# Kernel optimization log

Hardware: AMD Instinct MI355X
Metric: run time of the kernel (lower is better)

## Reference

```python
import jax, jax.numpy as jnp
import numpy as np

NUM_CLASSES = 345
EPS = 1e-12  # torch F.normalize eps


def setup_inputs() -> dict:
    key = jax.random.key(0)
    k1, k2, k3, k4 = jax.random.split(key, 4)
    B, D, N, C = 65536, 512, 34500, NUM_CLASSES
    z = jax.random.normal(k1, (B, D), dtype=jnp.float32)
    supports = jax.random.normal(k2, (N, D), dtype=jnp.float32)
    ent = jax.random.uniform(k3, (N,), dtype=jnp.float32)
    y_hat = jax.random.randint(k4, (N,), 0, C, dtype=jnp.int32)
    return {"z": z, "supports": supports, "ent": ent, "y_hat": y_hat, "filter_K": 100}


def reference(z, supports, ent, y_hat, filter_K):
    # Per-class top-filter_K selection by lowest entropy, expressed as a mask:
    # globally stable-sort by entropy, then per-class running count via one-hot cumsum.
    C = NUM_CLASSES
    order = jnp.argsort(ent)                      # stable sort -> matches per-class torch.sort tie-break
    y_sorted = y_hat[order]                       # [N]
    onehot = jax.nn.one_hot(y_sorted, C, dtype=z.dtype)  # [N, C]
    # rank (1-based, within own class) of each sorted support
    rank = jnp.sum(jnp.cumsum(onehot, axis=0) * onehot, axis=1)  # [N]
    sel = (rank <= filter_K).astype(z.dtype)      # [N] selection mask

    sup = supports[order]                         # [N, D]
    sup = sup / jnp.maximum(jnp.linalg.norm(sup, axis=1, keepdims=True), EPS)  # row-normalize
    # weights = selected_supports^T @ selected_labels (selection folded into mask)
    weights = jnp.einsum('nd,nc->dc', sup, onehot * sel[:, None])  # [D, C]
    weights = weights / jnp.maximum(jnp.linalg.norm(weights, axis=0, keepdims=True), EPS)
    return z @ weights                            # [B, C]
```

## Files before the change

### kernel.cpp

```cpp
#include <hip/hip_runtime.h>
#include <hip/hip_bf16.h>

#define NCLS 345
#define CPAD 384
#define DIM  512
#define BCAP 256

typedef float f32x4 __attribute__((ext_vector_type(4)));
typedef short s16x8 __attribute__((ext_vector_type(8)));
typedef short s16x4 __attribute__((ext_vector_type(4)));
typedef unsigned long long u64;

__device__ __forceinline__ short f2bf(float f) {
  union { float f; unsigned u; } v; v.f = f;
  unsigned r = v.u + 0x7fffu + ((v.u >> 16) & 1u);
  return (short)(r >> 16);
}

__global__ __launch_bounds__(256) void scan_classes(
    const float* __restrict__ ent, const int* __restrict__ y_hat,
    u64* __restrict__ bucket, int* __restrict__ cnt, int N)
{
  int i = blockIdx.x * 256 + threadIdx.x;
  if (i >= N) return;
  int c = y_hat[i];
  unsigned eb = __float_as_uint(ent[i]);
  u64 key = ((u64)eb << 32) | (unsigned)i;
  int p = atomicAdd(&cnt[c], 1);
  if (p < BCAP) bucket[(size_t)c * BCAP + p] = key;
}

__global__ __launch_bounds__(512) void select_accum(
    const float* __restrict__ supports, const u64* __restrict__ bucket,
    const int* __restrict__ cnt, const int* __restrict__ fKp,
    short* __restrict__ Wp)
{
  const int c = blockIdx.x;
  const int tid = threadIdx.x;
  const int lane = tid & 63, w = tid >> 6;
  __shared__ u64   s_key[BCAP];
  __shared__ int   s_selidx[BCAP];
  __shared__ int   s_nsel;
  __shared__ float s_part[8][DIM];
  __shared__ float s_red[8];
  if (tid == 0) s_nsel = 0;
  const int S = (c < NCLS) ? min(cnt[c], BCAP) : 0;
  const int K = fKp[0];
  for (int e = tid; e < S; e += 512) s_key[e] = bucket[(size_t)c * BCAP + e];
  __syncthreads();
  for (int e = tid; e < S; e += 512) {
    u64 ke = s_key[e];
    int r = 0;
    for (int j = 0; j < S; ++j) r += (s_key[j] < ke) ? 1 : 0;
    if (r < K) { int p = atomicAdd(&s_nsel, 1); s_selidx[p] = (int)(unsigned)(ke & 0xffffffffull); }
  }
  __syncthreads();
  const int nsel = s_nsel;
  f32x4 p0 = {0.f,0.f,0.f,0.f}, p1 = {0.f,0.f,0.f,0.f};
  for (int e0 = w; e0 < nsel; e0 += 16) {
    const int e1 = e0 + 8;
    const bool h1 = (e1 < nsel);
    const f32x4* r0 = (const f32x4*)(supports + (size_t)s_selidx[e0] * DIM);
    f32x4 a0 = r0[lane], a1 = r0[lane + 64];
    f32x4 b0 = {0.f,0.f,0.f,0.f}, b1 = {0.f,0.f,0.f,0.f};
    if (h1) {
      const f32x4* r1 = (const f32x4*)(supports + (size_t)s_selidx[e1] * DIM);
      b0 = r1[lane]; b1 = r1[lane + 64];
    }
    float s0 = 0.f, s1 = 0.f;
#pragma unroll
    for (int j = 0; j < 4; ++j) {
      s0 = fmaf(a0[j], a0[j], s0); s0 = fmaf(a1[j], a1[j], s0);
      s1 = fmaf(b0[j], b0[j], s1); s1 = fmaf(b1[j], b1[j], s1);
    }
#pragma unroll
    for (int off = 32; off; off >>= 1) { s0 += __shfl_xor(s0, off); s1 += __shfl_xor(s1, off); }
    float c0 = 1.f / fmaxf(sqrtf(s0), 1e-12f);
    float c1 = 1.f / fmaxf(sqrtf(s1), 1e-12f);
#pragma unroll
    for (int j = 0; j < 4; ++j) { p0[j] = fmaf(a0[j], c0, p0[j]); p1[j] = fmaf(a1[j], c0, p1[j]); }
    if (h1) {
#pragma unroll
      for (int j = 0; j < 4; ++j) { p0[j] = fmaf(b0[j], c1, p0[j]); p1[j] = fmaf(b1[j], c1, p1[j]); }
    }
  }
  *(f32x4*)&s_part[w][lane * 4]       = p0;
  *(f32x4*)&s_part[w][256 + lane * 4] = p1;
  __syncthreads();
  float acc = 0.f;
#pragma unroll
  for (int ww = 0; ww < 8; ++ww) acc += s_part[ww][tid];
  float sq = acc * acc;
#pragma unroll
  for (int off = 32; off; off >>= 1) sq += __shfl_xor(sq, off);
  if (lane == 0) s_red[w] = sq;
  __syncthreads();
  float tot = 0.f;
#pragma unroll
  for (int ww = 0; ww < 8; ++ww) tot += s_red[ww];
  float sc = 1.f / fmaxf(sqrtf(tot), 1e-12f);
  {
    const int k = tid;
    const int kt = k >> 5, fq = (k >> 3) & 3, j = k & 7;
    const int ct = c >> 4, fr = c & 15;
    const size_t pos = (size_t)(kt * 24 + ct) * 512 + fq * 128 + fr * 8 + j;
    Wp[pos] = f2bf(acc * sc);
  }
}

__global__ __launch_bounds__(512, 4) void gemm_zw(
    const float* __restrict__ z, const short* __restrict__ Wp,
    float* __restrict__ out)
{
  __shared__ __align__(16) char lds[65536];
  const int tid  = threadIdx.x;
  const int lane = tid & 63;
  const int w    = tid >> 6;
  const int fr   = lane & 15, fq = lane >> 4;
  const int Mbase = blockIdx.x * 64;

#pragma unroll
  for (int i = 0; i < 8; ++i) {
    const int row = i * 8 + w;
    const char* src = (const char*)(z + (size_t)(Mbase + row) * DIM);
    f32x4 v0 = *(const f32x4*)(src + lane * 16);
    f32x4 v1 = *(const f32x4*)(src + 1024 + lane * 16);
    s16x4 b0, b1;
#pragma unroll
    for (int j = 0; j < 4; ++j) { b0[j] = f2bf(v0[j]); b1[j] = f2bf(v1[j]); }
    const unsigned so = ((unsigned)(lane >> 1) ^ ((unsigned)row & 7)) * 16 + (lane & 1) * 8;
    *(s16x4*)(lds + row * 1024 + so)       = b0;
    *(s16x4*)(lds + row * 1024 + 512 + so) = b1;
  }
  __syncthreads();

  const char* pb = (const char*)Wp + (size_t)w * 3 * 1024 + (size_t)lane * 16;

  f32x4 acc[4][3];
#pragma unroll
  for (int mt = 0; mt < 4; ++mt)
#pragma unroll
    for (int nt = 0; nt < 3; ++nt) acc[mt][nt] = f32x4{0.f, 0.f, 0.f, 0.f};

  s16x8 Bbuf[2][3];
#pragma unroll
  for (int nt = 0; nt < 3; ++nt) Bbuf[0][nt] = *(const s16x8*)(pb + nt * 1024);

#pragma unroll
  for (int t = 0; t < 16; ++t) {
    const int p = t & 1;
    if (t < 15) {
#pragma unroll
      for (int nt = 0; nt < 3; ++nt)
        Bbuf[p ^ 1][nt] = *(const s16x8*)(pb + (size_t)(t + 1) * 24576 + nt * 1024);
    }
    s16x8 af[4];
#pragma unroll
    for (int mt = 0; mt < 4; ++mt) {
      const int row = mt * 16 + fr;
      const unsigned slot = ((unsigned)(t * 4) + fq) ^ ((unsigned)row & 7);
      af[mt] = *(const s16x8*)(lds + row * 1024 + slot * 16);
    }
    __builtin_amdgcn_s_setprio(1);
#pragma unroll
    for (int nt = 0; nt < 3; ++nt)
#pragma unroll
      for (int mt = 0; mt < 4; ++mt)
        acc[mt][nt] = __builtin_amdgcn_mfma_f32_16x16x32_bf16(Bbuf[p][nt], af[mt], acc[mt][nt], 0, 0, 0);
    __builtin_amdgcn_s_setprio(0);
  }

#pragma unroll
  for (int h = 0; h < 2; ++h) {
    __syncthreads();
#pragma unroll
    for (int ml = 0; ml < 2; ++ml) {
      const int mt = h * 2 + ml;
      const int rl = ml * 16 + fr;
#pragma unroll
      for (int nt = 0; nt < 3; ++nt) {
        const int colb = w * 48 + nt * 16 + fq * 4;
#pragma unroll
        for (int j = 0; j < 4; ++j) {
          const int col = colb + j;
          if (col < NCLS)
            *(float*)(lds + (((size_t)rl * NCLS + col) << 2)) = acc[mt][nt][j];
        }
      }
    }
    __syncthreads();
    char* dst = (char*)(out + (size_t)(Mbase + h * 32) * NCLS);
    for (int c = tid; c < 2760; c += 512) {
      f32x4 v = *(const f32x4*)(lds + c * 16);
      __builtin_nontemporal_store(v, (f32x4*)(dst + c * 16));
    }
  }
}

extern "C" void kernel_launch(void* const* d_in, const int* in_sizes, int n_in,
                              void* d_out, int out_size, void* d_ws, size_t ws_size,
                              hipStream_t stream) {
  const float* z        = (const float*)d_in[0];
  const float* supports = (const float*)d_in[1];
  const float* ent      = (const float*)d_in[2];
  const int*   y_hat    = (const int*)d_in[3];
  const int*   fK       = (const int*)d_in[4];
  float* out = (float*)d_out;
  short* Wp  = (short*)d_ws;
  const int N = in_sizes[2];
  const int M = in_sizes[0] / DIM;

  const size_t offC = (size_t)CPAD * DIM * 2;
  const size_t offB = offC + 2048;
  int* cnt    = (int*)((char*)d_ws + offC);
  u64* bucket = (u64*)((char*)d_ws + offB);
  hipMemsetAsync(cnt, 0, CPAD * sizeof(int), stream);
  scan_classes<<<dim3((N + 255) / 256), dim3(256), 0, stream>>>(ent, y_hat, bucket, cnt, N);
  select_accum<<<dim3(CPAD), dim3(512), 0, stream>>>(supports, bucket, cnt, fK, Wp);
  gemm_zw<<<dim3(M / 64), dim3(512), 0, stream>>>(z, Wp, out);
}
```

Measured before the change: 78.75 us.

## Stream GEMM B tiles into LDS triple buffer via global_load_lds

Loads of the packed weight tiles in the z@W GEMM are changed from register double-buffering to direct global-to-LDS loads (global_load_lds) into a per-wave triple buffer. Explicit vmcnt waits and sched barriers keep two tiles in flight. The goal is to free VGPRs and overlap B fetches with MFMA work. The cost is LDS use rising to about 136 KB per block and the 4-wave min-occupancy hint being removed, so the CU can hold fewer resident blocks to hide the memory-bound z read and output write.

```diff
diff --git a/kernel.cpp b/kernel.cpp
--- a/kernel.cpp
+++ b/kernel.cpp
@@ -108,11 +108,13 @@
   }
 }
 
-__global__ __launch_bounds__(512, 4) void gemm_zw(
+__global__ __launch_bounds__(512) void gemm_zw(
     const float* __restrict__ z, const short* __restrict__ Wp,
     float* __restrict__ out)
 {
-  __shared__ __align__(16) char lds[65536];
+  __shared__ __align__(16) char lds[139264];
+  char* const lA = lds;
+  char* const lB = lds + 65536;
   const int tid  = threadIdx.x;
   const int lane = tid & 63;
   const int w    = tid >> 6;
@@ -129,12 +131,28 @@
 #pragma unroll
     for (int j = 0; j < 4; ++j) { b0[j] = f2bf(v0[j]); b1[j] = f2bf(v1[j]); }
     const unsigned so = ((unsigned)(lane >> 1) ^ ((unsigned)row & 7)) * 16 + (lane & 1) * 8;
-    *(s16x4*)(lds + row * 1024 + so)       = b0;
-    *(s16x4*)(lds + row * 1024 + 512 + so) = b1;
-  }
-  __syncthreads();
-
-  const char* pb = (const char*)Wp + (size_t)w * 3 * 1024 + (size_t)lane * 16;
+    *(s16x4*)(lA + row * 1024 + so)       = b0;
+    *(s16x4*)(lA + row * 1024 + 512 + so) = b1;
+  }
+
+  const char* gB = (const char*)Wp + (size_t)w * 3 * 1024 + (size_t)lane * 16;
+  char* const myB = lB + w * 9216;
+
+#define ISSUE_B(T)                                                               \
+  {                                                                              \
+    _Pragma("unroll")                                                            \
+    for (int nt = 0; nt < 3; ++nt)                                               \
+      __builtin_amdgcn_global_load_lds(                                          \
+          (const __attribute__((address_space(1))) unsigned int*)                \
+              (gB + (size_t)(T) * 24576 + nt * 1024),                            \
+          (__attribute__((address_space(3))) unsigned int*)                      \
+              (myB + ((T) % 3) * 3072 + nt * 1024),                              \
+          16, 0, 0);                                                             \
+  }
+
+  ISSUE_B(0);
+  ISSUE_B(1);
+  __syncthreads();
 
   f32x4 acc[4][3];
 #pragma unroll
@@ -142,33 +160,34 @@
 #pragma unroll
     for (int nt = 0; nt < 3; ++nt) acc[mt][nt] = f32x4{0.f, 0.f, 0.f, 0.f};
 
-  s16x8 Bbuf[2][3];
-#pragma unroll
-  for (int nt = 0; nt < 3; ++nt) Bbuf[0][nt] = *(const s16x8*)(pb + nt * 1024);
-
 #pragma unroll
   for (int t = 0; t < 16; ++t) {
-    const int p = t & 1;
-    if (t < 15) {
-#pragma unroll
-      for (int nt = 0; nt < 3; ++nt)
-        Bbuf[p ^ 1][nt] = *(const s16x8*)(pb + (size_t)(t + 1) * 24576 + nt * 1024);
-    }
+    if (t + 2 < 16) ISSUE_B(t + 2);
+    __builtin_amdgcn_sched_barrier(0);
+    if (t <= 13)      asm volatile("s_waitcnt vmcnt(6)" ::: "memory");
+    else if (t == 14) asm volatile("s_waitcnt vmcnt(3)" ::: "memory");
+    else              asm volatile("s_waitcnt vmcnt(0)" ::: "memory");
+    __builtin_amdgcn_sched_barrier(0);
+    s16x8 bf[3];
+#pragma unroll
+    for (int nt = 0; nt < 3; ++nt)
+      bf[nt] = *(const s16x8*)(myB + (t % 3) * 3072 + nt * 1024 + lane * 16);
     s16x8 af[4];
 #pragma unroll
     for (int mt = 0; mt < 4; ++mt) {
       const int row = mt * 16 + fr;
       const unsigned slot = ((unsigned)(t * 4) + fq) ^ ((unsigned)row & 7);
-      af[mt] = *(const s16x8*)(lds + row * 1024 + slot * 16);
+      af[mt] = *(const s16x8*)(lA + row * 1024 + slot * 16);
     }
     __builtin_amdgcn_s_setprio(1);
 #pragma unroll
     for (int nt = 0; nt < 3; ++nt)
 #pragma unroll
       for (int mt = 0; mt < 4; ++mt)
-        acc[mt][nt] = __builtin_amdgcn_mfma_f32_16x16x32_bf16(Bbuf[p][nt], af[mt], acc[mt][nt], 0, 0, 0);
+        acc[mt][nt] = __builtin_amdgcn_mfma_f32_16x16x32_bf16(bf[nt], af[mt], acc[mt][nt], 0, 0, 0);
     __builtin_amdgcn_s_setprio(0);
   }
+#undef ISSUE_B
 
 #pragma unroll
   for (int h = 0; h < 2; ++h) {
@@ -184,14 +203,14 @@
         for (int j = 0; j < 4; ++j) {
           const int col = colb + j;
           if (col < NCLS)
-            *(float*)(lds + (((size_t)rl * NCLS + col) << 2)) = acc[mt][nt][j];
+            *(float*)(lA + (((size_t)rl * NCLS + col) << 2)) = acc[mt][nt][j];
         }
       }
     }
     __syncthreads();
     char* dst = (char*)(out + (size_t)(Mbase + h * 32) * NCLS);
     for (int c = tid; c < 2760; c += 512) {
-      f32x4 v = *(const f32x4*)(lds + c * 16);
+      f32x4 v = *(const f32x4*)(lA + c * 16);
       __builtin_nontemporal_store(v, (f32x4*)(dst + c * 16));
     }
   }
```

Measured after the change: 91.84 us. 16.6% more time.
